# Performance work log

Measured on AMD Instinct MI355X. Metric: run time of the kernel, lower is better.

## Reference

```python
import jax, jax.numpy as jnp
import numpy as np

EPS = 1e-12
ATTEND_SCALE = 8.0

def _l2norm(t, axis=-1):
    n = jnp.sqrt(jnp.sum(t * t, axis=axis, keepdims=True))
    return t / jnp.maximum(n, EPS)

def setup_inputs() -> dict:
    key = jax.random.key(0)
    k1, k2, k3, k4 = jax.random.split(key, 4)
    b, n, dim = 4, 8192, 1024
    heads, dim_head = 16, 64
    dim_inner = heads * dim_head
    x = jax.random.normal(k1, (b, n, dim), dtype=jnp.float32)
    gamma = jnp.ones((dim,), dtype=jnp.float32)  # RMSNorm gamma
    # torch Linear(dim, 3*dim_inner, bias=False): store as [dim, 3*dim_inner] for x @ W
    w_qkv = jax.random.normal(k2, (dim, 3 * dim_inner), dtype=jnp.float32) * (dim ** -0.5)
    temperature = jnp.zeros((heads, 1, 1), dtype=jnp.float32)
    w_out = jax.random.normal(k3, (dim_inner, dim), dtype=jnp.float32) * (dim_inner ** -0.5)
    return {"x": x, "gamma": gamma, "w_qkv": w_qkv, "temperature": temperature, "w_out": w_out}

def reference(x, gamma, w_qkv, temperature, w_out):
    b, n, dim = x.shape
    heads = temperature.shape[0]
    dim_head = w_qkv.shape[1] // (3 * heads)
    # RMSNorm: F.normalize(x, dim=-1) * sqrt(dim) * gamma
    xn = _l2norm(x) * (dim ** 0.5) * gamma
    qkv = xn @ w_qkv  # [b, n, 3*h*d]
    qkv = qkv.reshape(b, n, 3, heads, dim_head).transpose(2, 0, 3, 4, 1)  # [3, b, h, d, n]
    q, k, v = qkv[0], qkv[1], qkv[2]
    orig_v = v
    # l2-normalize q, k over the sequence axis (last dim of [b,h,d,n])
    q = _l2norm(q) * jnp.exp(temperature)  # temperature [h,1,1] broadcasts
    k = _l2norm(k)
    # attention over the feature axis: sim [b, h, d, d]
    sim = jnp.einsum('bhdn,bhen->bhde', q, k) * ATTEND_SCALE
    attn = jax.nn.softmax(sim, axis=-1)
    out = jnp.einsum('bhde,bhen->bhdn', attn, v)  # [b, h, d, n]
    out = out.transpose(0, 3, 1, 2).reshape(b, n, heads * dim_head) @ w_out  # [b, n, dim]
    return out, orig_v
```

## Files before the change

kernel.cpp:

```cpp
#include <hip/hip_runtime.h>
#include <hip/hip_bf16.h>

#define DEVI __device__ __forceinline__

using bf16x8 = __attribute__((ext_vector_type(8))) __bf16;
using f32x4  = __attribute__((ext_vector_type(4))) float;
using u16x8  = __attribute__((ext_vector_type(8))) unsigned short;

DEVI unsigned short f2bf(float f) {
  unsigned int u = __float_as_uint(f);
  u = (u + 0x7FFFu + ((u >> 16) & 1u)) >> 16;
  return (unsigned short)u;
}
DEVI float bf2f(unsigned short s) { return __uint_as_float(((unsigned int)s) << 16); }

DEVI void gld_lds16(const unsigned short* g, unsigned short* l) {
  __builtin_amdgcn_global_load_lds(
      (const __attribute__((address_space(1))) void*)g,
      (__attribute__((address_space(3))) void*)l, 16, 0, 0);
}

__global__ __launch_bounds__(256) void transpose_cast_kernel(const float* __restrict__ in,
                                                             unsigned short* __restrict__ out,
                                                             int R, int C) {
  __shared__ float tile[32][33];
  const int c0 = blockIdx.x * 32, r0 = blockIdx.y * 32;
  const int tx = threadIdx.x & 31, ty = threadIdx.x >> 5;
  for (int rr = ty; rr < 32; rr += 8)
    tile[rr][tx] = in[(size_t)(r0 + rr) * C + c0 + tx];
  __syncthreads();
  for (int cc = ty; cc < 32; cc += 8)
    out[(size_t)(c0 + cc) * R + r0 + tx] = f2bf(tile[tx][cc]);
}

__global__ __launch_bounds__(256) void castv_kernel(const float* __restrict__ w_qkv,
                                                    unsigned short* __restrict__ Wv_nt) {
  const int i = blockIdx.x * 256 + threadIdx.x;
  const int k = i >> 8, he4 = (i & 255) * 4;
  const float4 v = *(const float4*)&w_qkv[(size_t)k * 3072 + 2048 + he4];
  ushort4 o;
  o.x = f2bf(v.x); o.y = f2bf(v.y); o.z = f2bf(v.z); o.w = f2bf(v.w);
  *(ushort4*)&Wv_nt[(size_t)k * 1024 + he4] = o;
}

__global__ __launch_bounds__(256) void transpose_bf16x4_kernel(const unsigned short* __restrict__ in,
                                                               unsigned short* __restrict__ out) {
  __shared__ unsigned short tile[64][68];
  const int r0 = blockIdx.x * 64;
  const int c0 = blockIdx.y * 64;
  const int t = threadIdx.x;
  const int tr = t >> 4, tc4 = (t & 15) * 4;
#pragma unroll
  for (int p = 0; p < 4; ++p) {
    const int rr = p * 16 + tr;
    *(ushort4*)&tile[rr][tc4] = *(const ushort4*)&in[(size_t)(r0 + rr) * 1024 + c0 + tc4];
  }
  __syncthreads();
#pragma unroll
  for (int p = 0; p < 4; ++p) {
    const int cc = p * 16 + tr;
    ushort4 o;
    o.x = tile[tc4 + 0][cc];
    o.y = tile[tc4 + 1][cc];
    o.z = tile[tc4 + 2][cc];
    o.w = tile[tc4 + 3][cc];
    *(ushort4*)&out[(size_t)(c0 + cc) * 32768 + r0 + tc4] = o;
  }
}

__global__ __launch_bounds__(256) void rmsnorm_kernel(const float* __restrict__ x,
                                                      const float* __restrict__ gamma,
                                                      unsigned short* __restrict__ xn) {
  __shared__ float wsum[4];
  const int row = blockIdx.x;
  const int t = threadIdx.x;
  const float4 v = *(const float4*)&x[(size_t)row * 1024 + t * 4];
  float s = v.x * v.x + v.y * v.y + v.z * v.z + v.w * v.w;
  for (int off = 32; off; off >>= 1) s += __shfl_down(s, off);
  if ((t & 63) == 0) wsum[t >> 6] = s;
  __syncthreads();
  const float tot = wsum[0] + wsum[1] + wsum[2] + wsum[3];
  const float scale = 32.0f / fmaxf(sqrtf(tot), 1e-12f);
  const float4 g = *(const float4*)&gamma[t * 4];
  ushort4 o;
  o.x = f2bf(v.x * scale * g.x);
  o.y = f2bf(v.y * scale * g.y);
  o.z = f2bf(v.z * scale * g.z);
  o.w = f2bf(v.w * scale * g.w);
  *(ushort4*)&xn[(size_t)row * 1024 + t * 4] = o;
}

DEVI void stage256(const unsigned short* __restrict__ gA,
                   const unsigned short* __restrict__ gB,
                   unsigned short* lA, unsigned short* lB,
                   int k0, int w, int lane, size_t gstride) {
  const int dr = lane >> 3;
  const int ks = (lane & 7) ^ dr;
  const size_t lo = (size_t)dr * gstride + k0 + ks * 8;
#pragma unroll
  for (int i = 0; i < 4; ++i) {
    const int oct = w * 4 + i;
    gld_lds16(gA + (size_t)oct * 8 * gstride + lo, lA + oct * 512 + lane * 8);
    gld_lds16(gB + (size_t)oct * 8 * gstride + lo, lB + oct * 512 + lane * 8);
  }
}

DEVI void compute256(const unsigned short* __restrict__ lA,
                     const unsigned short* __restrict__ lB,
                     int wm, int wn, int lane, f32x4 (&acc)[8][4]) {
  const int r = lane & 15, kg = lane >> 4;
  const int r7 = r & 7;
#pragma unroll
  for (int ksl = 0; ksl < 2; ++ksl) {
    const int sA = (((ksl << 2) + kg) ^ r7) * 8;
    bf16x8 af[8], bfr[4];
#pragma unroll
    for (int m = 0; m < 8; ++m)
      af[m] = *(const bf16x8*)&lA[(wm * 128 + m * 16 + r) * 64 + sA];
#pragma unroll
    for (int n = 0; n < 4; ++n)
      bfr[n] = *(const bf16x8*)&lB[(wn * 64 + n * 16 + r) * 64 + sA];
#pragma unroll
    for (int m = 0; m < 8; ++m)
#pragma unroll
      for (int n = 0; n < 4; ++n)
        acc[m][n] = __builtin_amdgcn_mfma_f32_16x16x32_bf16(af[m], bfr[n], acc[m][n], 0, 0, 0);
  }
}

#define VOUT_BAR()  __builtin_amdgcn_sched_barrier(0); __builtin_amdgcn_s_barrier(); \
                    __builtin_amdgcn_sched_barrier(0)
#define VOUT_W8()   asm volatile("s_waitcnt vmcnt(8)" ::: "memory")
#define VOUT_W0()   asm volatile("s_waitcnt vmcnt(0)" ::: "memory")

__global__ __launch_bounds__(512, 2) void gemm_gram256_kernel(
    const unsigned short* __restrict__ xnT, unsigned short* __restrict__ Gp) {
  if (blockIdx.x > blockIdx.y) return;
  __shared__ __align__(16) unsigned short Al[2][16384];
  __shared__ __align__(16) unsigned short Bl[2][16384];
  const int tid = threadIdx.x;
  const int lane = tid & 63;
  const int w = tid >> 6;
  const int wm = w >> 2, wn = w & 3;
  const int z = blockIdx.z;
  const size_t koff = (size_t)(z >> 2) * 8192 + (size_t)(z & 3) * 2048;
  const unsigned short* gA = xnT + (size_t)blockIdx.y * 256 * 32768 + koff;
  const unsigned short* gB = xnT + (size_t)blockIdx.x * 256 * 32768 + koff;

  f32x4 acc[8][4] = {};
  stage256(gA, gB, Al[0], Bl[0], 0, w, lane, 32768);
#pragma unroll 1
  for (int tt = 0; tt < 15; ++tt) {
    stage256(gA, gB, Al[1], Bl[1], (tt * 2 + 1) * 64, w, lane, 32768);
    VOUT_W8(); VOUT_BAR();
    __builtin_amdgcn_s_setprio(1);
    compute256(Al[0], Bl[0], wm, wn, lane, acc);
    __builtin_amdgcn_s_setprio(0);
    VOUT_BAR();
    stage256(gA, gB, Al[0], Bl[0], (tt * 2 + 2) * 64, w, lane, 32768);
    VOUT_W8(); VOUT_BAR();
    __builtin_amdgcn_s_setprio(1);
    compute256(Al[1], Bl[1], wm, wn, lane, acc);
    __builtin_amdgcn_s_setprio(0);
    VOUT_BAR();
  }
  stage256(gA, gB, Al[1], Bl[1], 31 * 64, w, lane, 32768);
  VOUT_W8(); VOUT_BAR();
  __builtin_amdgcn_s_setprio(1);
  compute256(Al[0], Bl[0], wm, wn, lane, acc);
  __builtin_amdgcn_s_setprio(0);
  VOUT_BAR();
  VOUT_W0(); VOUT_BAR();
  __builtin_amdgcn_s_setprio(1);
  compute256(Al[1], Bl[1], wm, wn, lane, acc);
  __builtin_amdgcn_s_setprio(0);

  unsigned short* C = Gp + ((size_t)z << 20);
  const int rr = (lane >> 4) * 4;
  const int cc = lane & 15;
  const size_t grow0 = (size_t)blockIdx.y * 256 + wm * 128;
  const int gc0 = blockIdx.x * 256 + wn * 64;
#pragma unroll
  for (int m = 0; m < 8; ++m)
#pragma unroll
    for (int n = 0; n < 4; ++n)
#pragma unroll
      for (int j = 0; j < 4; ++j)
        C[(grow0 + m * 16 + rr + j) * 1024 + gc0 + n * 16 + cc] = f2bf(acc[m][n][j]);
}

__global__ __launch_bounds__(256) void greduce_kernel(const unsigned short* __restrict__ Gp,
                                                      unsigned short* __restrict__ G) {
  const int tj = blockIdx.x, ti = blockIdx.y, b = blockIdx.z;
  if ((tj >> 2) > (ti >> 2)) return;
  __shared__ float lds[64][65];
  const int t = threadIdx.x;
  const int r = t >> 2, c0 = (t & 3) * 16;
  const size_t idx = (size_t)(ti * 64 + r) * 1024 + tj * 64 + c0;
  float v[16];
#pragma unroll
  for (int j = 0; j < 16; ++j) v[j] = 0.f;
  for (int s = 0; s < 4; ++s) {
    const unsigned short* p = Gp + ((size_t)(b * 4 + s) << 20) + idx;
#pragma unroll
    for (int j = 0; j < 16; ++j) v[j] += bf2f(p[j]);
  }
  unsigned short* Gb = G + ((size_t)b << 20);
  __attribute__((aligned(16))) unsigned short buf[16];
#pragma unroll
  for (int j = 0; j < 16; ++j) buf[j] = f2bf(v[j]);
  { int4* dst = (int4*)&Gb[idx]; const int4* src = (const int4*)buf; dst[0] = src[0]; dst[1] = src[1]; }
  if ((ti >> 2) != (tj >> 2)) {
#pragma unroll
    for (int j = 0; j < 16; ++j) lds[r][c0 + j] = v[j];
    __syncthreads();
    const int x = t >> 2, y0 = (t & 3) * 16;
#pragma unroll
    for (int j = 0; j < 16; ++j) buf[j] = f2bf(lds[y0 + j][x]);
    int4* dst = (int4*)&Gb[(size_t)(tj * 64 + x) * 1024 + ti * 64 + y0];
    const int4* src = (const int4*)buf;
    dst[0] = src[0]; dst[1] = src[1];
  }
}

__global__ __launch_bounds__(256) void gemm_bt_batch_bf16(const unsigned short* __restrict__ A,
                                                          const unsigned short* __restrict__ Bt,
                                                          unsigned short* __restrict__ C,
                                                          int N, int K,
                                                          long long aStr, long long bStr, long long cStr) {
  __shared__ __align__(16) unsigned short Al[4096];
  __shared__ __align__(16) unsigned short Bl[4096];
  A += (size_t)blockIdx.z * aStr; Bt += (size_t)blockIdx.z * bStr; C += (size_t)blockIdx.z * cStr;
  const int tid = threadIdx.x;
  const int lane = tid & 63, wid = tid >> 6;
  const int wr = wid >> 1, wc = wid & 1;
  const int r = lane & 15, kg = lane >> 4;
  const int rw0 = tid >> 2, q0 = (tid & 3) * 8;
  const size_t row0 = (size_t)blockIdx.y * 128, col0 = (size_t)blockIdx.x * 128;
  f32x4 acc[4][4] = {};
  for (int k0 = 0; k0 < K; k0 += 32) {
    __syncthreads();
    gld_lds16(&A[(row0 + rw0) * K + k0 + q0], &Al[tid * 8]);
    gld_lds16(&A[(row0 + rw0 + 64) * K + k0 + q0], &Al[2048 + tid * 8]);
    gld_lds16(&Bt[(col0 + rw0) * K + k0 + q0], &Bl[tid * 8]);
    gld_lds16(&Bt[(col0 + rw0 + 64) * K + k0 + q0], &Bl[2048 + tid * 8]);
    __syncthreads();
    bf16x8 af[4], bfr[4];
#pragma unroll
    for (int m = 0; m < 4; ++m) af[m] = *(const bf16x8*)&Al[(wr * 64 + m * 16 + r) * 32 + kg * 8];
#pragma unroll
    for (int n = 0; n < 4; ++n) bfr[n] = *(const bf16x8*)&Bl[(wc * 64 + n * 16 + r) * 32 + kg * 8];
#pragma unroll
    for (int m = 0; m < 4; ++m)
#pragma unroll
      for (int n = 0; n < 4; ++n)
        acc[m][n] = __builtin_amdgcn_mfma_f32_16x16x32_bf16(af[m], bfr[n], acc[m][n], 0, 0, 0);
  }
  const int rbase = wr * 64 + (lane >> 4) * 4;
  const int cbase = wc * 64 + (lane & 15);
#pragma unroll
  for (int m = 0; m < 4; ++m)
#pragma unroll
    for (int n = 0; n < 4; ++n)
#pragma unroll
      for (int j = 0; j < 4; ++j)
        C[(row0 + rbase + m * 16 + j) * N + col0 + cbase + n * 16] = f2bf(acc[m][n][j]);
}

__global__ __launch_bounds__(512, 2) void gemm_vout256_kernel(
    const unsigned short* __restrict__ A,
    const unsigned short* __restrict__ BtV,
    const unsigned short* __restrict__ WfoldT,
    float* __restrict__ origv,
    float* __restrict__ outp) {
  __shared__ __align__(16) unsigned short Al[2][16384];
  __shared__ __align__(16) unsigned short Bl[2][16384];
  const int tid = threadIdx.x;
  const int lane = tid & 63;
  const int w = tid >> 6;
  const int wm = w >> 2, wn = w & 3;
  const int xcd = blockIdx.x & 7;
  const int j = blockIdx.x >> 3;
  const int rb = xcd * 16 + (j >> 3);
  const int cb = j & 7;
  const int b = rb >> 5;
  const unsigned short* gA = A + (size_t)rb * 256 * 1024;
  const unsigned short* gB = (cb < 4)
      ? BtV + (size_t)cb * 256 * 1024
      : WfoldT + ((size_t)b << 20) + (size_t)(cb - 4) * 256 * 1024;

  f32x4 acc[8][4] = {};
  stage256(gA, gB, Al[0], Bl[0], 0, w, lane, 1024);
#pragma unroll 1
  for (int tt = 0; tt < 7; ++tt) {
    stage256(gA, gB, Al[1], Bl[1], (tt * 2 + 1) * 64, w, lane, 1024);
    VOUT_W8(); VOUT_BAR();
    __builtin_amdgcn_s_setprio(1);
    compute256(Al[0], Bl[0], wm, wn, lane, acc);
    __builtin_amdgcn_s_setprio(0);
    VOUT_BAR();
    stage256(gA, gB, Al[0], Bl[0], (tt * 2 + 2) * 64, w, lane, 1024);
    VOUT_W8(); VOUT_BAR();
    __builtin_amdgcn_s_setprio(1);
    compute256(Al[1], Bl[1], wm, wn, lane, acc);
    __builtin_amdgcn_s_setprio(0);
    VOUT_BAR();
  }
  stage256(gA, gB, Al[1], Bl[1], 15 * 64, w, lane, 1024);
  VOUT_W8(); VOUT_BAR();
  __builtin_amdgcn_s_setprio(1);
  compute256(Al[0], Bl[0], wm, wn, lane, acc);
  __builtin_amdgcn_s_setprio(0);
  VOUT_BAR();
  VOUT_W0(); VOUT_BAR();
  __builtin_amdgcn_s_setprio(1);
  compute256(Al[1], Bl[1], wm, wn, lane, acc);
  __builtin_amdgcn_s_setprio(0);

  const int rr = (lane >> 4) * 4;
  const int cc = lane & 15;
  if (cb < 4) {
    const int nbase = (rb & 31) * 256 + wm * 128;
#pragma unroll
    for (int m = 0; m < 8; ++m)
#pragma unroll
      for (int n = 0; n < 4; ++n) {
        const int hd = cb * 256 + wn * 64 + n * 16 + cc;
        const float4 o4 = make_float4(acc[m][n][0], acc[m][n][1], acc[m][n][2], acc[m][n][3]);
        *(float4*)&origv[((size_t)b * 1024 + hd) * 8192 + nbase + m * 16 + rr] = o4;
      }
  } else {
    const size_t grow0 = (size_t)rb * 256 + wm * 128;
    const int gc0 = (cb - 4) * 256 + wn * 64;
#pragma unroll
    for (int m = 0; m < 8; ++m)
#pragma unroll
      for (int n = 0; n < 4; ++n)
#pragma unroll
        for (int j2 = 0; j2 < 4; ++j2)
          outp[(grow0 + m * 16 + rr + j2) * 1024 + gc0 + n * 16 + cc] = acc[m][n][j2];
  }
}

__global__ __launch_bounds__(256) void norms_kernel(const unsigned short* __restrict__ UTt,
                                                    const unsigned short* __restrict__ wqkvT,
                                                    float* __restrict__ qkn2) {
  const int t = threadIdx.x;
  const int rloc = t >> 4, lane16 = t & 15;
  const int row = blockIdx.x * 16 + rloc;
  const int b = row >> 11, r2 = row & 2047;
  const unsigned short* pa = UTt + ((size_t)b << 21) + (size_t)r2 * 1024 + lane16 * 64;
  const unsigned short* pb = wqkvT + (size_t)r2 * 1024 + lane16 * 64;
  float s = 0.f;
  for (int i = 0; i < 64; i += 8) {
    const u16x8 va = *(const u16x8*)&pa[i];
    const u16x8 vb = *(const u16x8*)&pb[i];
#pragma unroll
    for (int j = 0; j < 8; ++j) s += bf2f(va[j]) * bf2f(vb[j]);
  }
  for (int off = 8; off; off >>= 1) s += __shfl_down(s, off, 16);
  if (lane16 == 0) qkn2[row] = s;
}

__global__ __launch_bounds__(256) void sim_softmax_kernel(const unsigned short* __restrict__ wqkvT,
                                                          const unsigned short* __restrict__ UTt,
                                                          const float* __restrict__ qkn2,
                                                          const float* __restrict__ temperature,
                                                          float* __restrict__ attn) {
  __shared__ __align__(16) unsigned short Aql[64 * 128];
  __shared__ __align__(16) unsigned short Bkl[64 * 128];
  __shared__ float qknl[2][64];
  const int bh = blockIdx.x;
  const int b = bh >> 4, h = bh & 15;
  const int t = threadIdx.x;
  const int lane = t & 63, w = t >> 6;
  const unsigned short* UTtb = UTt + ((size_t)b << 21);
  if (t < 128) {
    const int sel = t >> 6, dd = t & 63;
    qknl[sel][dd] = fmaxf(sqrtf(qkn2[b * 2048 + sel * 1024 + h * 64 + dd]), 1e-12f);
  }
  const unsigned short* AqG = UTtb + (size_t)(h * 64) * 1024;
  const unsigned short* BkG = wqkvT + (size_t)(1024 + h * 64) * 1024;
  const int r = lane & 15, kg = lane >> 4;
  const int srow = t >> 4, scol = (t & 15) * 8;
  f32x4 acc[4] = {};
  for (int k0 = 0; k0 < 1024; k0 += 128) {
    __syncthreads();
#pragma unroll
    for (int c = 0; c < 4; ++c) {
      gld_lds16(&AqG[(size_t)(c * 16 + srow) * 1024 + k0 + scol], &Aql[c * 2048 + t * 8]);
      gld_lds16(&BkG[(size_t)(c * 16 + srow) * 1024 + k0 + scol], &Bkl[c * 2048 + t * 8]);
    }
    __syncthreads();
#pragma unroll
    for (int kk = 0; kk < 128; kk += 32) {
      const bf16x8 af = *(const bf16x8*)&Aql[(w * 16 + r) * 128 + kk + kg * 8];
#pragma unroll
      for (int n = 0; n < 4; ++n) {
        const bf16x8 bfr = *(const bf16x8*)&Bkl[(n * 16 + r) * 128 + kk + kg * 8];
        acc[n] = __builtin_amdgcn_mfma_f32_16x16x32_bf16(af, bfr, acc[n], 0, 0, 0);
      }
    }
  }
  const float sc = 8.f * __expf(temperature[h]);
  const int colq = lane & 15, rq = lane >> 4;
#pragma unroll
  for (int j = 0; j < 4; ++j) {
    const int d = w * 16 + rq * 4 + j;
    const float qd = qknl[0][d];
    float sv[4];
#pragma unroll
    for (int n = 0; n < 4; ++n) sv[n] = acc[n][j] * sc / (qd * qknl[1][n * 16 + colq]);
    float mj = fmaxf(fmaxf(sv[0], sv[1]), fmaxf(sv[2], sv[3]));
    for (int msk = 1; msk < 16; msk <<= 1) mj = fmaxf(mj, __shfl_xor(mj, msk));
    float p[4], sum = 0.f;
#pragma unroll
    for (int n = 0; n < 4; ++n) { p[n] = __expf(sv[n] - mj); sum += p[n]; }
    for (int msk = 1; msk < 16; msk <<= 1) sum += __shfl_xor(sum, msk);
    const float inv = 1.f / sum;
#pragma unroll
    for (int n = 0; n < 4; ++n)
      attn[(size_t)bh * 4096 + d * 64 + n * 16 + colq] = p[n] * inv;
  }
}

__global__ __launch_bounds__(256) void w2t_kernel(const float* __restrict__ attn,
                                                  const float* __restrict__ w_out,
                                                  unsigned short* __restrict__ W2T) {
  __shared__ float al[64][64];
  __shared__ float wl[64][64];
  const int bh = blockIdx.y;
  const int b = bh >> 4, h = bh & 15;
  const int c0 = blockIdx.x * 256;
  const int t = threadIdx.x, e = t & 63, g = t >> 6;
  const int dr = t >> 2, q4 = (t & 3) * 16;
#pragma unroll
  for (int j = 0; j < 16; j += 4)
    *(float4*)&al[dr][q4 + j] = *(const float4*)&attn[(size_t)bh * 4096 + dr * 64 + q4 + j];
  for (int cbk = 0; cbk < 4; ++cbk) {
    __syncthreads();
#pragma unroll
    for (int j = 0; j < 16; j += 4)
      *(float4*)&wl[dr][q4 + j] = *(const float4*)&w_out[(size_t)(h * 64 + dr) * 1024 + c0 + cbk * 64 + q4 + j];
    __syncthreads();
#pragma unroll
    for (int i = 0; i < 16; ++i) {
      const int cc = g * 16 + i;
      float s = 0.f;
#pragma unroll 8
      for (int d = 0; d < 64; ++d) s += al[d][e] * wl[d][cc];
      W2T[((size_t)b << 20) + (size_t)(c0 + cbk * 64 + cc) * 1024 + h * 64 + e] = f2bf(s);
    }
  }
}

extern "C" void kernel_launch(void* const* d_in, const int* in_sizes, int n_in,
                              void* d_out, int out_size, void* d_ws, size_t ws_size,
                              hipStream_t stream) {
  const float* x     = (const float*)d_in[0];
  const float* gamma = (const float*)d_in[1];
  const float* w_qkv = (const float*)d_in[2];
  const float* temp  = (const float*)d_in[3];
  const float* w_out = (const float*)d_in[4];
  char* ws = (char*)d_ws;
  unsigned short* wqkvT  = (unsigned short*)(ws);
  unsigned short* Wv_nt  = (unsigned short*)(ws + 6291456);
  unsigned short* xn     = (unsigned short*)(ws + 8388608);
  unsigned short* xnT    = (unsigned short*)(ws + 75497472);
  unsigned short* Gp     = (unsigned short*)(ws + 142606336);
  unsigned short* G      = (unsigned short*)(ws + 176160768);
  unsigned short* UTt    = (unsigned short*)(ws + 184549376);
  float* qkn2            = (float*)(ws + 201326592);
  float* attn            = (float*)(ws + 201359360);
  unsigned short* W2T    = (unsigned short*)(ws + 202407936);
  unsigned short* WfoldT = (unsigned short*)(ws + 210796544);
  float* outp  = (float*)d_out;
  float* origv = outp + (size_t)33554432;

  transpose_cast_kernel<<<dim3(96, 32), 256, 0, stream>>>(w_qkv, wqkvT, 1024, 3072);
  castv_kernel<<<1024, 256, 0, stream>>>(w_qkv, Wv_nt);
  rmsnorm_kernel<<<32768, 256, 0, stream>>>(x, gamma, xn);
  transpose_bf16x4_kernel<<<dim3(512, 16), 256, 0, stream>>>(xn, xnT);
  gemm_gram256_kernel<<<dim3(4, 4, 16), 512, 0, stream>>>(xnT, Gp);
  greduce_kernel<<<dim3(16, 16, 4), 256, 0, stream>>>(Gp, G);
  gemm_bt_batch_bf16<<<dim3(8, 16, 4), 256, 0, stream>>>(wqkvT, G, UTt, 1024, 1024,
                                                         0LL, 1LL << 20, 1LL << 21);
  norms_kernel<<<512, 256, 0, stream>>>(UTt, wqkvT, qkn2);
  sim_softmax_kernel<<<64, 256, 0, stream>>>(wqkvT, UTt, qkn2, temp, attn);
  w2t_kernel<<<dim3(4, 64), 256, 0, stream>>>(attn, w_out, W2T);
  gemm_bt_batch_bf16<<<dim3(8, 8, 4), 256, 0, stream>>>(W2T, Wv_nt, WfoldT, 1024, 1024,
                                                        1LL << 20, 0LL, 1LL << 20);
  gemm_vout256_kernel<<<1024, 512, 0, stream>>>(xn, wqkvT + (size_t)2048 * 1024, WfoldT,
                                                origv, outp);
}
```

Baseline: 478.1 us.

## Fuse RMSNorm with transpose and compact gram grid with XCD-aware tile mapping

Merges the RMSNorm kernel and the bf16 transpose into one kernel that normalizes 64 rows into a large LDS tile and writes both the row-major and transposed outputs, so the transpose no longer rereads xn from global memory. The gram GEMM now launches only the 160 lower-triangular tiles via a lookup table and maps blocks so that each XCD handles a single split-K slice, instead of launching 256 blocks and exiting the upper-triangle ones early. The fused kernel runs only 512 blocks with about 128KB of LDS each, which limits occupancy. Its transposed writes are 128-byte rows per thread built through a per-thread LDS gather.

```diff
diff --git a/kernel.cpp b/kernel.cpp
--- a/kernel.cpp
+++ b/kernel.cpp
@@ -43,51 +43,51 @@
   *(ushort4*)&Wv_nt[(size_t)k * 1024 + he4] = o;
 }
 
-__global__ __launch_bounds__(256) void transpose_bf16x4_kernel(const unsigned short* __restrict__ in,
-                                                               unsigned short* __restrict__ out) {
-  __shared__ unsigned short tile[64][68];
+__global__ __launch_bounds__(512) void rmsnorm_t_kernel(const float* __restrict__ x,
+                                                        const float* __restrict__ gamma,
+                                                        unsigned short* __restrict__ xn,
+                                                        unsigned short* __restrict__ xnT) {
+  __shared__ unsigned short tile[64][1028];
   const int r0 = blockIdx.x * 64;
-  const int c0 = blockIdx.y * 64;
   const int t = threadIdx.x;
-  const int tr = t >> 4, tc4 = (t & 15) * 4;
-#pragma unroll
-  for (int p = 0; p < 4; ++p) {
-    const int rr = p * 16 + tr;
-    *(ushort4*)&tile[rr][tc4] = *(const ushort4*)&in[(size_t)(r0 + rr) * 1024 + c0 + tc4];
+  const int wv = t >> 6, lane = t & 63;
+#pragma unroll 1
+  for (int p = 0; p < 8; ++p) {
+    const int rr = p * 8 + wv;
+    const size_t base = (size_t)(r0 + rr) * 1024;
+    float4 v[4];
+    float s = 0.f;
+#pragma unroll
+    for (int q = 0; q < 4; ++q) {
+      v[q] = *(const float4*)&x[base + q * 256 + lane * 4];
+      s += v[q].x * v[q].x + v[q].y * v[q].y + v[q].z * v[q].z + v[q].w * v[q].w;
+    }
+    for (int off = 32; off; off >>= 1) s += __shfl_down(s, off);
+    s = __shfl(s, 0);
+    const float scale = 32.0f / fmaxf(sqrtf(s), 1e-12f);
+#pragma unroll
+    for (int q = 0; q < 4; ++q) {
+      const int c = q * 256 + lane * 4;
+      const float4 g = *(const float4*)&gamma[c];
+      ushort4 o;
+      o.x = f2bf(v[q].x * scale * g.x);
+      o.y = f2bf(v[q].y * scale * g.y);
+      o.z = f2bf(v[q].z * scale * g.z);
+      o.w = f2bf(v[q].w * scale * g.w);
+      *(ushort4*)&xn[base + c] = o;
+      *(ushort4*)&tile[rr][c] = o;
+    }
   }
   __syncthreads();
-#pragma unroll
-  for (int p = 0; p < 4; ++p) {
-    const int cc = p * 16 + tr;
-    ushort4 o;
-    o.x = tile[tc4 + 0][cc];
-    o.y = tile[tc4 + 1][cc];
-    o.z = tile[tc4 + 2][cc];
-    o.w = tile[tc4 + 3][cc];
-    *(ushort4*)&out[(size_t)(c0 + cc) * 32768 + r0 + tc4] = o;
-  }
-}
-
-__global__ __launch_bounds__(256) void rmsnorm_kernel(const float* __restrict__ x,
-                                                      const float* __restrict__ gamma,
-                                                      unsigned short* __restrict__ xn) {
-  __shared__ float wsum[4];
-  const int row = blockIdx.x;
-  const int t = threadIdx.x;
-  const float4 v = *(const float4*)&x[(size_t)row * 1024 + t * 4];
-  float s = v.x * v.x + v.y * v.y + v.z * v.z + v.w * v.w;
-  for (int off = 32; off; off >>= 1) s += __shfl_down(s, off);
-  if ((t & 63) == 0) wsum[t >> 6] = s;
-  __syncthreads();
-  const float tot = wsum[0] + wsum[1] + wsum[2] + wsum[3];
-  const float scale = 32.0f / fmaxf(sqrtf(tot), 1e-12f);
-  const float4 g = *(const float4*)&gamma[t * 4];
-  ushort4 o;
-  o.x = f2bf(v.x * scale * g.x);
-  o.y = f2bf(v.y * scale * g.y);
-  o.z = f2bf(v.z * scale * g.z);
-  o.w = f2bf(v.w * scale * g.w);
-  *(ushort4*)&xn[(size_t)row * 1024 + t * 4] = o;
+  for (int cc = t; cc < 1024; cc += 512) {
+    __attribute__((aligned(16))) unsigned short buf[64];
+#pragma unroll
+    for (int r = 0; r < 64; ++r) buf[r] = tile[r][cc];
+    int4* dst = (int4*)&xnT[(size_t)cc * 32768 + r0];
+    const int4* src = (const int4*)buf;
+#pragma unroll
+    for (int q = 0; q < 8; ++q) dst[q] = src[q];
+  }
 }
 
 DEVI void stage256(const unsigned short* __restrict__ gA,
@@ -133,19 +133,26 @@
 #define VOUT_W8()   asm volatile("s_waitcnt vmcnt(8)" ::: "memory")
 #define VOUT_W0()   asm volatile("s_waitcnt vmcnt(0)" ::: "memory")
 
+__constant__ int g_txl[10] = {0, 0, 1, 0, 1, 2, 0, 1, 2, 3};
+__constant__ int g_tyl[10] = {0, 1, 1, 2, 2, 2, 3, 3, 3, 3};
+
 __global__ __launch_bounds__(512, 2) void gemm_gram256_kernel(
     const unsigned short* __restrict__ xnT, unsigned short* __restrict__ Gp) {
-  if (blockIdx.x > blockIdx.y) return;
   __shared__ __align__(16) unsigned short Al[2][16384];
   __shared__ __align__(16) unsigned short Bl[2][16384];
+  const int blk = blockIdx.x;
+  const int xcd = blk & 7;
+  const int seq = blk >> 3;
+  const int z = xcd + 8 * (seq / 10);
+  const int tl = seq % 10;
+  const int bx = g_txl[tl], by = g_tyl[tl];
   const int tid = threadIdx.x;
   const int lane = tid & 63;
   const int w = tid >> 6;
   const int wm = w >> 2, wn = w & 3;
-  const int z = blockIdx.z;
   const size_t koff = (size_t)(z >> 2) * 8192 + (size_t)(z & 3) * 2048;
-  const unsigned short* gA = xnT + (size_t)blockIdx.y * 256 * 32768 + koff;
-  const unsigned short* gB = xnT + (size_t)blockIdx.x * 256 * 32768 + koff;
+  const unsigned short* gA = xnT + (size_t)by * 256 * 32768 + koff;
+  const unsigned short* gB = xnT + (size_t)bx * 256 * 32768 + koff;
 
   f32x4 acc[8][4] = {};
   stage256(gA, gB, Al[0], Bl[0], 0, w, lane, 32768);
@@ -178,8 +185,8 @@
   unsigned short* C = Gp + ((size_t)z << 20);
   const int rr = (lane >> 4) * 4;
   const int cc = lane & 15;
-  const size_t grow0 = (size_t)blockIdx.y * 256 + wm * 128;
-  const int gc0 = blockIdx.x * 256 + wn * 64;
+  const size_t grow0 = (size_t)by * 256 + wm * 128;
+  const int gc0 = bx * 256 + wn * 64;
 #pragma unroll
   for (int m = 0; m < 8; ++m)
 #pragma unroll
@@ -479,9 +486,8 @@
 
   transpose_cast_kernel<<<dim3(96, 32), 256, 0, stream>>>(w_qkv, wqkvT, 1024, 3072);
   castv_kernel<<<1024, 256, 0, stream>>>(w_qkv, Wv_nt);
-  rmsnorm_kernel<<<32768, 256, 0, stream>>>(x, gamma, xn);
-  transpose_bf16x4_kernel<<<dim3(512, 16), 256, 0, stream>>>(xn, xnT);
-  gemm_gram256_kernel<<<dim3(4, 4, 16), 512, 0, stream>>>(xnT, Gp);
+  rmsnorm_t_kernel<<<512, 512, 0, stream>>>(x, gamma, xn, xnT);
+  gemm_gram256_kernel<<<160, 512, 0, stream>>>(xnT, Gp);
   greduce_kernel<<<dim3(16, 16, 4), 256, 0, stream>>>(Gp, G);
   gemm_bt_batch_bf16<<<dim3(8, 16, 4), 256, 0, stream>>>(wqkvT, G, UTt, 1024, 1024,
                                                          0LL, 1LL << 20, 1LL << 21);
```

Measured after the change: 486.2 us. About the same (+1.7%).

## Replace double-buffered LDS pipeline with single-buffer synchronous staging in vout GEMM

Applied to the files above, without the earlier changes.

The V/out GEMM kernel drops its two-stage LDS double buffer, where the next K-tile was loaded asynchronously while the current one was computed. It now uses one buffer: barrier, stage the tile, barrier, compute, repeated 16 times. This halves the LDS footprint, which could let more blocks fit per CU, but global-to-LDS loads no longer overlap with MFMA compute. Each iteration now waits on a full barrier for its own load.

```diff
diff --git a/kernel.cpp b/kernel.cpp
--- a/kernel.cpp
+++ b/kernel.cpp
@@ -273,8 +273,8 @@
     const unsigned short* __restrict__ WfoldT,
     float* __restrict__ origv,
     float* __restrict__ outp) {
-  __shared__ __align__(16) unsigned short Al[2][16384];
-  __shared__ __align__(16) unsigned short Bl[2][16384];
+  __shared__ __align__(16) unsigned short Al[16384];
+  __shared__ __align__(16) unsigned short Bl[16384];
   const int tid = threadIdx.x;
   const int lane = tid & 63;
   const int w = tid >> 6;
@@ -290,32 +290,15 @@
       : WfoldT + ((size_t)b << 20) + (size_t)(cb - 4) * 256 * 1024;
 
   f32x4 acc[8][4] = {};
-  stage256(gA, gB, Al[0], Bl[0], 0, w, lane, 1024);
 #pragma unroll 1
-  for (int tt = 0; tt < 7; ++tt) {
-    stage256(gA, gB, Al[1], Bl[1], (tt * 2 + 1) * 64, w, lane, 1024);
-    VOUT_W8(); VOUT_BAR();
+  for (int t = 0; t < 16; ++t) {
+    __syncthreads();
+    stage256(gA, gB, Al, Bl, t * 64, w, lane, 1024);
+    __syncthreads();
     __builtin_amdgcn_s_setprio(1);
-    compute256(Al[0], Bl[0], wm, wn, lane, acc);
+    compute256(Al, Bl, wm, wn, lane, acc);
     __builtin_amdgcn_s_setprio(0);
-    VOUT_BAR();
-    stage256(gA, gB, Al[0], Bl[0], (tt * 2 + 2) * 64, w, lane, 1024);
-    VOUT_W8(); VOUT_BAR();
-    __builtin_amdgcn_s_setprio(1);
-    compute256(Al[1], Bl[1], wm, wn, lane, acc);
-    __builtin_amdgcn_s_setprio(0);
-    VOUT_BAR();
-  }
-  stage256(gA, gB, Al[1], Bl[1], 15 * 64, w, lane, 1024);
-  VOUT_W8(); VOUT_BAR();
-  __builtin_amdgcn_s_setprio(1);
-  compute256(Al[0], Bl[0], wm, wn, lane, acc);
-  __builtin_amdgcn_s_setprio(0);
-  VOUT_BAR();
-  VOUT_W0(); VOUT_BAR();
-  __builtin_amdgcn_s_setprio(1);
-  compute256(Al[1], Bl[1], wm, wn, lane, acc);
-  __builtin_amdgcn_s_setprio(0);
+  }
 
   const int rr = (lane >> 4) * 4;
   const int cc = lane & 15;
```

Result: slower. 496.7 us (+3.9%).
